# Kernel tuning notes

Measured on AMD Instinct MI355X. Metric: run time of the kernel, lower is better.

The kernel has to match this reference:

```python
import jax, jax.numpy as jnp
import numpy as np

ROPE_BASE = 10000.0


def _rope(x):
    # Faithful to the torch module: positions indexed by x.shape[2],
    # which after split_heads is the HEADS axis. x: [B, S, H, D]
    B, S, H, D = x.shape
    theta = 1.0 / (ROPE_BASE ** (jnp.arange(0, D, 2, dtype=x.dtype) / D))  # [D/2]
    pos = jnp.arange(H, dtype=x.dtype)[:, None]  # [H, 1]
    ang = pos * theta  # [H, D/2], broadcasts against [B, S, H, D/2]
    sin, cos = jnp.sin(ang), jnp.cos(ang)
    xe, xo = x[..., 0::2], x[..., 1::2]
    re = xe * cos - xo * sin
    ro = xe * sin + xo * cos
    # interleave back: even slots <- re, odd slots <- ro
    return jnp.stack([re, ro], axis=-1).reshape(B, S, H, D)


def setup_inputs() -> dict:
    key = jax.random.key(0)
    k0, k1, k2, k3 = jax.random.split(key, 4)
    B, S, Dm = 8, 2048, 2048
    scale = 1.0 / np.sqrt(Dm)
    return {
        "x": jax.random.normal(k0, (B, S, Dm), dtype=jnp.float32),
        "Wq": jax.random.normal(k1, (Dm, Dm), dtype=jnp.float32) * scale,
        "Wk": jax.random.normal(k2, (Dm, Dm), dtype=jnp.float32) * scale,
        "Wv": jax.random.normal(k3, (Dm, Dm), dtype=jnp.float32) * scale,
        "st_pos": 0,
    }


def reference(x, Wq, Wk, Wv, st_pos):
    B, S, Dm = x.shape
    H = 16
    D = Dm // H  # head_dim = 128
    q = jnp.einsum("bsd,df->bsf", x, Wq).reshape(B, S, H, D)
    k = jnp.einsum("bsd,df->bsf", x, Wk).reshape(B, S, H, D)
    v = jnp.einsum("bsd,df->bsf", x, Wv).reshape(B, S, H, D)
    q = _rope(q)
    k = _rope(k)
    return q, k, v
```

## Files before the change

### kernel.cpp

```cpp
#include <hip/hip_runtime.h>
#include <hip/hip_bf16.h>
#include <stdint.h>


typedef __attribute__((ext_vector_type(8))) short short8;
typedef __attribute__((ext_vector_type(4))) float f32x4;

__device__ __forceinline__ unsigned short f2bf(float f) {
  __bf16 h = (__bf16)f;
  return __builtin_bit_cast(unsigned short, h);
}

__device__ __forceinline__ void gload_lds16(const void* g, void* l) {
  __builtin_amdgcn_global_load_lds((const __attribute__((address_space(1))) void*)g,
                                   (__attribute__((address_space(3))) void*)l,
                                   16, 0, 0);
}


__global__ __launch_bounds__(256) void convert_x(const float* __restrict__ X,
                                                 unsigned short* __restrict__ Xb,
                                                 int n8) {
  const int stride = gridDim.x * blockDim.x;
  for (int i = blockIdx.x * blockDim.x + threadIdx.x; i < n8; i += stride) {
    const float4 v0 = ((const float4*)X)[(size_t)i * 2 + 0];
    const float4 v1 = ((const float4*)X)[(size_t)i * 2 + 1];
    uint4 w;
    w.x = (uint32_t)f2bf(v0.x) | ((uint32_t)f2bf(v0.y) << 16);
    w.y = (uint32_t)f2bf(v0.z) | ((uint32_t)f2bf(v0.w) << 16);
    w.z = (uint32_t)f2bf(v1.x) | ((uint32_t)f2bf(v1.y) << 16);
    w.w = (uint32_t)f2bf(v1.z) | ((uint32_t)f2bf(v1.w) << 16);
    ((uint4*)Xb)[i] = w;
  }
}

__global__ __launch_bounds__(256) void transpose_cvt3(const float* __restrict__ W0,
                                                      const float* __restrict__ W1,
                                                      const float* __restrict__ W2,
                                                      unsigned short* __restrict__ WT) {
  __shared__ unsigned short tile[64][65];
  const int z = blockIdx.z;
  const float* W = (z == 0) ? W0 : (z == 1) ? W1 : W2;
  unsigned short* WTz = WT + (size_t)z * 2048 * 2048;
  const int bx = blockIdx.x * 64;
  const int by = blockIdx.y * 64;
  const int t  = threadIdx.x;
  const int tr = t >> 4;
  const int tc = (t & 15) * 4;
#pragma unroll
  for (int i = 0; i < 4; ++i) {
    const int r = tr + i * 16;
    const float4 v = *(const float4*)&W[(size_t)(by + r) * 2048 + bx + tc];
    tile[r][tc + 0] = f2bf(v.x);
    tile[r][tc + 1] = f2bf(v.y);
    tile[r][tc + 2] = f2bf(v.z);
    tile[r][tc + 3] = f2bf(v.w);
  }
  __syncthreads();
#pragma unroll
  for (int i = 0; i < 4; ++i) {
    const int a = tr + i * 16;
    ushort4 o;
    o.x = tile[tc + 0][a];
    o.y = tile[tc + 1][a];
    o.z = tile[tc + 2][a];
    o.w = tile[tc + 3][a];
    *(ushort4*)&WTz[(size_t)(bx + a) * 2048 + by + tc] = o;
  }
}


__global__ __launch_bounds__(512, 2) void qkv_fused15(const unsigned short* __restrict__ Xb,
                                                      const unsigned short* __restrict__ WT,
                                                      float* __restrict__ Out) {
  extern __shared__ char smem[];

  const int wg  = blockIdx.x;
  const int swz = (wg & 7) * 192 + (wg >> 3);
  const int mb  = swz / 24, nb = swz % 24;
  const int m0  = mb * 256, n0 = nb * 256;

  const int tid  = threadIdx.x;
  const int wave = tid >> 6, lane = tid & 63;
  const int l15  = lane & 15, lg = lane >> 4;
  const int wm   = (wave >> 2) * 128;
  const int wn   = (wave & 3) * 64;
  const int s0   = ((lg ^ (l15 & 7)) << 4);

  const unsigned short* Xp = Xb + (size_t)m0 * 2048;
  const unsigned short* Wp = WT + (size_t)n0 * 2048;

  const int srow  = tid >> 3;
  const int sslot = tid & 7;

  f32x4 acc[8][4] = {};

#define GLD_A(TP1)                                                            \
  do {                                                                        \
    char* dst_ = smem + (((TP1) & 1) << 16);                                  \
    _Pragma("unroll") for (int i_ = 0; i_ < 4; ++i_) {                        \
      const int row_ = i_ * 64 + srow;                                        \
      gload_lds16(Xp + (size_t)row_ * 2048 + (TP1) * 64 +                     \
                      ((sslot ^ (row_ & 7)) << 3),                            \
                  dst_ + i_ * 8192 + tid * 16);                               \
    }                                                                         \
  } while (0)

#define GLD_B(TP2, H)                                                         \
  do {                                                                        \
    char* dst_ = smem + (((TP2) & 1) << 16) + 32768 + ((H) << 14);            \
    _Pragma("unroll") for (int i_ = 0; i_ < 2; ++i_) {                        \
      const int row_ = (H) * 128 + i_ * 64 + srow;                            \
      gload_lds16(Wp + (size_t)row_ * 2048 + (TP2) * 64 +                     \
                      ((sslot ^ (row_ & 7)) << 3),                            \
                  dst_ + i_ * 8192 + tid * 16);                               \
    }                                                                         \
  } while (0)

#define LDA4(DST, MH, KS)                                                     \
  _Pragma("unroll") for (int mi_ = 0; mi_ < 4; ++mi_)                         \
      (DST)[mi_] = *(const short8*)(Ab +                                      \
          ((wm + (MH) * 64 + mi_ * 16 + l15) << 7) + (s0 ^ ((KS) << 6)));

#define LDB4(DST, KS)                                                         \
  _Pragma("unroll") for (int ni_ = 0; ni_ < 4; ++ni_)                         \
      (DST)[ni_] = *(const short8*)(Bb +                                      \
          ((wn + ni_ * 16 + l15) << 7) + (s0 ^ ((KS) << 6)));

#define MFMA16(MH, AR, BR)                                                    \
  do {                                                                        \
    __builtin_amdgcn_s_setprio(1);                                            \
    _Pragma("unroll") for (int mi_ = 0; mi_ < 4; ++mi_)                       \
      _Pragma("unroll") for (int ni_ = 0; ni_ < 4; ++ni_)                     \
        asm("v_mfma_f32_16x16x32_bf16 %0, %1, %2, %0"                         \
            : "+v"(acc[(MH) * 4 + mi_][ni_])                                  \
            : "v"((AR)[mi_]), "v"((BR)[ni_]));                                \
    __builtin_amdgcn_s_setprio(0);                                            \
  } while (0)

  GLD_A(0);
  GLD_B(0, 0); GLD_B(0, 1);
  GLD_B(1, 0); GLD_B(1, 1);
  asm volatile("s_waitcnt vmcnt(4)" ::: "memory");
  __builtin_amdgcn_s_barrier();

  for (int t = 0; t < 32; ++t) {
    const char* Ab = smem + ((t & 1) << 16);
    const char* Bb = Ab + 32768;
    short8 a0[4], a1[4], b0[4], b1[4];

    if (t < 31) GLD_A(t + 1);
    LDB4(b0, 0);
    LDA4(a0, 0, 0);
    LDA4(a1, 1, 0);
    MFMA16(0, a0, b0);
    LDB4(b1, 1);
    LDA4(a0, 0, 1);
    MFMA16(1, a1, b0);
    asm volatile("s_waitcnt lgkmcnt(0)" ::: "memory");
    __builtin_amdgcn_s_barrier();
    if (t < 30) { GLD_B(t + 2, 0); GLD_B(t + 2, 1); }
    LDA4(a1, 1, 1);
    MFMA16(0, a0, b1);
    MFMA16(1, a1, b1);
    if (t == 30)     asm volatile("s_waitcnt vmcnt(0)" ::: "memory");
    else if (t < 30) asm volatile("s_waitcnt vmcnt(4)" ::: "memory");
    if (t < 31) __builtin_amdgcn_s_barrier();
  }

#undef GLD_A
#undef GLD_B
#undef LDA4
#undef LDB4
#undef MFMA16

#pragma unroll
  for (int ni = 0; ni < 4; ++ni) {
    const int col = n0 + wn + ni * 16 + l15;
    const int sec = col >> 11;
    const int lc  = col & 2047;
    float c = 1.0f, ssg = 0.0f;
    if (sec < 2) {
      const int h = lc >> 7;
      const int p = (lc & 127) >> 1;
      const float theta = exp2f(-(float)p * 0.20762050593046014f);
      float s;
      sincosf((float)h * theta, &s, &c);
      ssg = (l15 & 1) ? s : -s;
    }
    float* outp = Out + (size_t)sec * 33554432 + lc;
#pragma unroll
    for (int mi = 0; mi < 8; ++mi) {
      const f32x4 a = acc[mi][ni];
#pragma unroll
      for (int r = 0; r < 4; ++r) {
        const float val = a[r];
        float res = val;
        if (sec < 2) {
          const float other = __shfl_xor(val, 1);
          res = val * c + other * ssg;
        }
        __builtin_nontemporal_store(
            res, outp + (size_t)(m0 + wm + mi * 16 + lg * 4 + r) * 2048);
      }
    }
  }
}

__global__ __launch_bounds__(256) void qkv_gemm_small(const float* __restrict__ X,
                                                      const unsigned short* __restrict__ WTl,
                                                      float* __restrict__ Out,
                                                      const int do_rope) {
  __shared__ unsigned short As[128 * 64];
  __shared__ unsigned short Bs[128 * 64];
  const int t    = threadIdx.x;
  const int wave = t >> 6, lane = t & 63;
  const int l15  = lane & 15, lg = lane >> 4;
  const int wm   = (wave >> 1) * 64;
  const int wn   = (wave & 1) * 64;
  const int m0   = blockIdx.y * 128;
  const int n0   = blockIdx.x * 128;

  f32x4 acc[4][4] = {};

  for (int kt = 0; kt < 2048; kt += 64) {
#pragma unroll
    for (int i = 0; i < 8; ++i) {
      const int f = i * 256 + t;
      const int row = f >> 4, chunk = f & 15;
      const float4 v = *(const float4*)&X[(size_t)(m0 + row) * 2048 + kt + chunk * 4];
      const uint32_t lo = (uint32_t)f2bf(v.x) | ((uint32_t)f2bf(v.y) << 16);
      const uint32_t hi = (uint32_t)f2bf(v.z) | ((uint32_t)f2bf(v.w) << 16);
      const int slot = chunk >> 1;
      const int off  = row * 128 + (((slot ^ (row & 7)) << 4) | ((chunk & 1) << 3));
      uint2* p = (uint2*)((char*)As + off);
      p->x = lo; p->y = hi;
    }
#pragma unroll
    for (int i = 0; i < 4; ++i) {
      const int seg = i * 4 + wave;
      const int row = seg * 8 + (lane >> 3);
      const int ps  = lane & 7;
      const int ss  = ps ^ (row & 7);
      gload_lds16(WTl + (size_t)(n0 + row) * 2048 + kt + ss * 8,
                  (char*)Bs + seg * 1024 + lane * 16);
    }
    __syncthreads();
#pragma unroll
    for (int kk = 0; kk < 2; ++kk) {
      short8 afr[4], bfr[4];
#pragma unroll
      for (int mi = 0; mi < 4; ++mi) {
        const int row  = wm + mi * 16 + l15;
        const int slot = kk * 4 + lg;
        afr[mi] = *(const short8*)((const char*)As + row * 128 + ((slot ^ (row & 7)) << 4));
      }
#pragma unroll
      for (int ni = 0; ni < 4; ++ni) {
        const int row  = wn + ni * 16 + l15;
        const int slot = kk * 4 + lg;
        bfr[ni] = *(const short8*)((const char*)Bs + row * 128 + ((slot ^ (row & 7)) << 4));
      }
#pragma unroll
      for (int mi = 0; mi < 4; ++mi)
#pragma unroll
        for (int ni = 0; ni < 4; ++ni)
          asm("v_mfma_f32_16x16x32_bf16 %0, %1, %2, %0"
              : "+v"(acc[mi][ni])
              : "v"(afr[mi]), "v"(bfr[ni]));
    }
    __syncthreads();
  }

#pragma unroll
  for (int ni = 0; ni < 4; ++ni) {
    const int col = n0 + wn + ni * 16 + l15;
    float c = 1.0f, ssg = 0.0f;
    if (do_rope) {
      const int h = col >> 7;
      const int p = (col & 127) >> 1;
      const float theta = exp2f(-(float)p * 0.20762050593046014f);
      float s;
      sincosf((float)h * theta, &s, &c);
      ssg = (l15 & 1) ? s : -s;
    }
#pragma unroll
    for (int mi = 0; mi < 4; ++mi) {
      const f32x4 a = acc[mi][ni];
#pragma unroll
      for (int r = 0; r < 4; ++r) {
        const float val = a[r];
        float res = val;
        if (do_rope) {
          const float other = __shfl_xor(val, 1);
          res = val * c + other * ssg;
        }
        Out[(size_t)(m0 + wm + mi * 16 + lg * 4 + r) * 2048 + col] = res;
      }
    }
  }
}

extern "C" void kernel_launch(void* const* d_in, const int* in_sizes, int n_in,
                              void* d_out, int out_size, void* d_ws, size_t ws_size,
                              hipStream_t stream) {
  (void)in_sizes; (void)n_in; (void)out_size;
  const float* x  = (const float*)d_in[0];
  const float* Wq = (const float*)d_in[1];
  const float* Wk = (const float*)d_in[2];
  const float* Wv = (const float*)d_in[3];
  float* out = (float*)d_out;

  const size_t XB_ELEMS = 16384ull * 2048;
  const size_t WT_ELEMS = 6144ull * 2048;

  if (ws_size >= (XB_ELEMS + WT_ELEMS) * sizeof(unsigned short)) {
    unsigned short* Xb  = (unsigned short*)d_ws;
    unsigned short* WTf = Xb + XB_ELEMS;
    convert_x<<<2048, 256, 0, stream>>>(x, Xb, (int)(XB_ELEMS / 8));
    transpose_cvt3<<<dim3(32, 32, 3), 256, 0, stream>>>(Wq, Wk, Wv, WTf);
    hipFuncSetAttribute((const void*)qkv_fused15,
                        hipFuncAttributeMaxDynamicSharedMemorySize, 131072);
    qkv_fused15<<<1536, 512, 131072, stream>>>(Xb, WTf, out);
  } else {
    unsigned short* WqT = (unsigned short*)d_ws;
    unsigned short* WkT = WqT + 2048ull * 2048;
    unsigned short* WvT = WkT + 2048ull * 2048;
    dim3 tb(256), tg(32, 32);
    transpose_cvt3<<<dim3(32, 32, 1), 256, 0, stream>>>(Wq, Wq, Wq, WqT);
    transpose_cvt3<<<dim3(32, 32, 1), 256, 0, stream>>>(Wk, Wk, Wk, WkT);
    transpose_cvt3<<<dim3(32, 32, 1), 256, 0, stream>>>(Wv, Wv, Wv, WvT);
    dim3 gg(16, 128);
    qkv_gemm_small<<<gg, tb, 0, stream>>>(x, WqT, out,            1);
    qkv_gemm_small<<<gg, tb, 0, stream>>>(x, WkT, out + 33554432, 1);
    qkv_gemm_small<<<gg, tb, 0, stream>>>(x, WvT, out + 67108864, 0);
  }
}
```

Measured before the change: 437.7 us.

## Split GEMM workgroup into 16 waves each owning a 64x64 sub-tile

The fused QKV GEMM workgroup grows from 512 to 1024 threads. Each wave now owns a 64x64 output sub-tile instead of 128x64, which halves the accumulator registers per wave. The global-to-LDS loads and the MFMA schedule are reorganised to match, with fewer loads per thread and a single B load per stage. The goal is more waves in flight to hide latency. In exchange, each LDS fragment is reused by fewer MFMAs, which raises LDS read traffic per flop. The launch bounds (1024, 4) may also force a tight register budget and cause spills.

```diff
diff --git a/kernel.cpp b/kernel.cpp
--- a/kernel.cpp
+++ b/kernel.cpp
@@ -70,9 +70,9 @@
 }
 
 
-__global__ __launch_bounds__(512, 2) void qkv_fused15(const unsigned short* __restrict__ Xb,
-                                                      const unsigned short* __restrict__ WT,
-                                                      float* __restrict__ Out) {
+__global__ __launch_bounds__(1024, 4) void qkv_fused16(const unsigned short* __restrict__ Xb,
+                                                       const unsigned short* __restrict__ WT,
+                                                       float* __restrict__ Out) {
   extern __shared__ char smem[];
 
   const int wg  = blockIdx.x;
@@ -83,7 +83,7 @@
   const int tid  = threadIdx.x;
   const int wave = tid >> 6, lane = tid & 63;
   const int l15  = lane & 15, lg = lane >> 4;
-  const int wm   = (wave >> 2) * 128;
+  const int wm   = (wave >> 2) * 64;
   const int wn   = (wave & 3) * 64;
   const int s0   = ((lg ^ (l15 & 7)) << 4);
 
@@ -93,78 +93,74 @@
   const int srow  = tid >> 3;
   const int sslot = tid & 7;
 
-  f32x4 acc[8][4] = {};
+  f32x4 acc[4][4] = {};
 
 #define GLD_A(TP1)                                                            \
   do {                                                                        \
     char* dst_ = smem + (((TP1) & 1) << 16);                                  \
-    _Pragma("unroll") for (int i_ = 0; i_ < 4; ++i_) {                        \
-      const int row_ = i_ * 64 + srow;                                        \
+    _Pragma("unroll") for (int i_ = 0; i_ < 2; ++i_) {                        \
+      const int row_ = i_ * 128 + srow;                                       \
       gload_lds16(Xp + (size_t)row_ * 2048 + (TP1) * 64 +                     \
                       ((sslot ^ (row_ & 7)) << 3),                            \
-                  dst_ + i_ * 8192 + tid * 16);                               \
+                  dst_ + i_ * 16384 + tid * 16);                              \
     }                                                                         \
   } while (0)
 
-#define GLD_B(TP2, H)                                                         \
+#define GLD_B(TP2)                                                            \
   do {                                                                        \
-    char* dst_ = smem + (((TP2) & 1) << 16) + 32768 + ((H) << 14);            \
+    char* dst_ = smem + (((TP2) & 1) << 16) + 32768;                          \
     _Pragma("unroll") for (int i_ = 0; i_ < 2; ++i_) {                        \
-      const int row_ = (H) * 128 + i_ * 64 + srow;                            \
+      const int row_ = i_ * 128 + srow;                                       \
       gload_lds16(Wp + (size_t)row_ * 2048 + (TP2) * 64 +                     \
                       ((sslot ^ (row_ & 7)) << 3),                            \
-                  dst_ + i_ * 8192 + tid * 16);                               \
+                  dst_ + i_ * 16384 + tid * 16);                              \
     }                                                                         \
   } while (0)
 
-#define LDA4(DST, MH, KS)                                                     \
+#define LDA4(DST, KS)                                                         \
   _Pragma("unroll") for (int mi_ = 0; mi_ < 4; ++mi_)                         \
       (DST)[mi_] = *(const short8*)(Ab +                                      \
-          ((wm + (MH) * 64 + mi_ * 16 + l15) << 7) + (s0 ^ ((KS) << 6)));
+          ((wm + mi_ * 16 + l15) << 7) + (s0 ^ ((KS) << 6)));
 
 #define LDB4(DST, KS)                                                         \
   _Pragma("unroll") for (int ni_ = 0; ni_ < 4; ++ni_)                         \
       (DST)[ni_] = *(const short8*)(Bb +                                      \
           ((wn + ni_ * 16 + l15) << 7) + (s0 ^ ((KS) << 6)));
 
-#define MFMA16(MH, AR, BR)                                                    \
+#define MFMA16(AR, BR)                                                        \
   do {                                                                        \
     __builtin_amdgcn_s_setprio(1);                                            \
     _Pragma("unroll") for (int mi_ = 0; mi_ < 4; ++mi_)                       \
       _Pragma("unroll") for (int ni_ = 0; ni_ < 4; ++ni_)                     \
         asm("v_mfma_f32_16x16x32_bf16 %0, %1, %2, %0"                         \
-            : "+v"(acc[(MH) * 4 + mi_][ni_])                                  \
+            : "+v"(acc[mi_][ni_])                                             \
             : "v"((AR)[mi_]), "v"((BR)[ni_]));                                \
     __builtin_amdgcn_s_setprio(0);                                            \
   } while (0)
 
   GLD_A(0);
-  GLD_B(0, 0); GLD_B(0, 1);
-  GLD_B(1, 0); GLD_B(1, 1);
-  asm volatile("s_waitcnt vmcnt(4)" ::: "memory");
+  GLD_B(0);
+  GLD_B(1);
+  asm volatile("s_waitcnt vmcnt(2)" ::: "memory");
   __builtin_amdgcn_s_barrier();
 
   for (int t = 0; t < 32; ++t) {
     const char* Ab = smem + ((t & 1) << 16);
     const char* Bb = Ab + 32768;
-    short8 a0[4], a1[4], b0[4], b1[4];
+    short8 a0[4], b0[4], a1[4], b1[4];
 
     if (t < 31) GLD_A(t + 1);
     LDB4(b0, 0);
-    LDA4(a0, 0, 0);
-    LDA4(a1, 1, 0);
-    MFMA16(0, a0, b0);
+    LDA4(a0, 0);
+    MFMA16(a0, b0);
     LDB4(b1, 1);
-    LDA4(a0, 0, 1);
-    MFMA16(1, a1, b0);
+    LDA4(a1, 1);
     asm volatile("s_waitcnt lgkmcnt(0)" ::: "memory");
     __builtin_amdgcn_s_barrier();
-    if (t < 30) { GLD_B(t + 2, 0); GLD_B(t + 2, 1); }
-    LDA4(a1, 1, 1);
-    MFMA16(0, a0, b1);
-    MFMA16(1, a1, b1);
+    if (t < 30) GLD_B(t + 2);
+    MFMA16(a1, b1);
     if (t == 30)     asm volatile("s_waitcnt vmcnt(0)" ::: "memory");
-    else if (t < 30) asm volatile("s_waitcnt vmcnt(4)" ::: "memory");
+    else if (t < 30) asm volatile("s_waitcnt vmcnt(2)" ::: "memory");
     if (t < 31) __builtin_amdgcn_s_barrier();
   }
 
@@ -190,7 +186,7 @@
     }
     float* outp = Out + (size_t)sec * 33554432 + lc;
 #pragma unroll
-    for (int mi = 0; mi < 8; ++mi) {
+    for (int mi = 0; mi < 4; ++mi) {
       const f32x4 a = acc[mi][ni];
 #pragma unroll
       for (int r = 0; r < 4; ++r) {
@@ -319,9 +315,9 @@
     unsigned short* WTf = Xb + XB_ELEMS;
     convert_x<<<2048, 256, 0, stream>>>(x, Xb, (int)(XB_ELEMS / 8));
     transpose_cvt3<<<dim3(32, 32, 3), 256, 0, stream>>>(Wq, Wk, Wv, WTf);
-    hipFuncSetAttribute((const void*)qkv_fused15,
+    hipFuncSetAttribute((const void*)qkv_fused16,
                         hipFuncAttributeMaxDynamicSharedMemorySize, 131072);
-    qkv_fused15<<<1536, 512, 131072, stream>>>(Xb, WTf, out);
+    qkv_fused16<<<1536, 1024, 131072, stream>>>(Xb, WTf, out);
   } else {
     unsigned short* WqT = (unsigned short*)d_ws;
     unsigned short* WkT = WqT + 2048ull * 2048;
```

Result: faster. 421.2 us (-3.8%).
